# Performance work log

Hardware: AMD Instinct MI355X
Metric: run time of the kernel (lower is better)

Reference implementation:

```python
import jax, jax.numpy as jnp
import numpy as np

N, D, H, TOPK = 1024, 128, 8, 16
HD = D // H
EPS = 1e-5


def _linear_init(key, fan_in, fan_out):
    lim = 1.0 / np.sqrt(fan_in)
    kw, kb = jax.random.split(key)
    W = jax.random.uniform(kw, (fan_in, fan_out), minval=-lim, maxval=lim, dtype=jnp.float32)
    b = jax.random.uniform(kb, (fan_out,), minval=-lim, maxval=lim, dtype=jnp.float32)
    return W, b


def setup_inputs() -> dict:
    key = jax.random.key(0)
    ks = jax.random.split(key, 16)
    h = jax.random.normal(ks[0], (N, D), dtype=jnp.float32)
    e = jax.random.normal(ks[1], (N, N, D), dtype=jnp.float32)
    adjm_bin = jax.random.randint(ks[2], (N, N), 0, 2, dtype=jnp.int32)
    Wq, bq = _linear_init(ks[3], D, D)
    Wk, bk = _linear_init(ks[4], D, D)
    Wv, bv = _linear_init(ks[5], D, D)
    We, be = _linear_init(ks[6], D, H)
    Wo, bo = _linear_init(ks[7], D, D)
    Wf1, bf1 = _linear_init(ks[8], D, 4 * D)
    Wf2, bf2 = _linear_init(ks[9], 4 * D, D)
    # torch LSTMCell layout: W_ih [4D, D], W_hh [4D, D], gate order i,f,g,o
    lim = 1.0 / np.sqrt(D)
    Wih = jax.random.uniform(ks[10], (4 * D, D), minval=-lim, maxval=lim, dtype=jnp.float32)
    Whh = jax.random.uniform(ks[11], (4 * D, D), minval=-lim, maxval=lim, dtype=jnp.float32)
    bih = jax.random.uniform(ks[12], (4 * D,), minval=-lim, maxval=lim, dtype=jnp.float32)
    bhh = jax.random.uniform(ks[13], (4 * D,), minval=-lim, maxval=lim, dtype=jnp.float32)
    gn_g = jnp.ones((D,), jnp.float32); gn_b = jnp.zeros((D,), jnp.float32)
    ln1_g = jnp.ones((D,), jnp.float32); ln1_b = jnp.zeros((D,), jnp.float32)
    ln2_g = jnp.ones((D,), jnp.float32); ln2_b = jnp.zeros((D,), jnp.float32)
    return dict(h=h, e=e, adjm_bin=adjm_bin, Wq=Wq, bq=bq, Wk=Wk, bk=bk, Wv=Wv, bv=bv,
                We=We, be=be, Wo=Wo, bo=bo, Wf1=Wf1, bf1=bf1, Wf2=Wf2, bf2=bf2,
                Wih=Wih, Whh=Whh, bih=bih, bhh=bhh, gn_g=gn_g, gn_b=gn_b,
                ln1_g=ln1_g, ln1_b=ln1_b, ln2_g=ln2_g, ln2_b=ln2_b)


def _layernorm(x, g, b):
    mu = jnp.mean(x, axis=-1, keepdims=True)
    var = jnp.var(x, axis=-1, keepdims=True)
    return g * (x - mu) * jax.lax.rsqrt(var + EPS) + b


def _forward(h, e, Wq, bq, Wk, bk, Wv, bv, We, be, Wo, bo, Wf1, bf1, Wf2, bf2,
             Wih, Whh, bih, bhh, gn_g, gn_b, ln1_g, ln1_b, ln2_g, ln2_b):
    n = h.shape[0]
    residual = h
    q = (h @ Wq + bq).reshape(n, H, HD)
    k = (h @ Wk + bk).reshape(n, H, HD)
    v = (h @ Wv + bv).reshape(n, H, HD)
    scores = jnp.einsum('ihd,jhd->ijh', q, k) / np.sqrt(HD).astype(np.float32)
    scores = scores + (e @ We + be)                      # [N, N, H]
    # per-head top-k over neighbor dim j (axis=1)
    s = scores.transpose(0, 2, 1)                        # [N, H, N]
    _, idx = jax.lax.top_k(s, TOPK)                      # [N, H, K]
    mask = jnp.zeros(s.shape, bool).at[
        jnp.arange(n)[:, None, None], jnp.arange(H)[None, :, None], idx].set(True)
    mask = mask.transpose(0, 2, 1)                       # [N, N, H]
    scores = jnp.where(mask, scores, -jnp.inf)
    attn = jax.nn.softmax(scores, axis=1)
    h_attn = jnp.einsum('ijh,jhd->ihd', attn, v).reshape(n, D)
    h_attn = h_attn @ Wo + bo
    x = _layernorm(residual + h_attn, ln1_g, ln1_b)
    # LSTMCell with zero initial state (memory_state=None branch)
    gates = x @ Wih.T + bih + jnp.zeros_like(x) @ Whh.T + bhh
    gi, gf, gg, go = jnp.split(gates, 4, axis=-1)
    i = jax.nn.sigmoid(gi); f = jax.nn.sigmoid(gf)
    g = jnp.tanh(gg); o = jax.nn.sigmoid(go)
    c_next = i * g                                       # f * 0 dropped
    h_next = o * jnp.tanh(c_next)
    x = x + h_next
    # GraphNorm: normalize over node dim 0
    mu = jnp.mean(x, axis=0, keepdims=True)
    var = jnp.var(x, axis=0, keepdims=True)
    x = gn_g * (x - mu) * jax.lax.rsqrt(var + EPS) + gn_b
    h_ffn = jax.nn.relu(x @ Wf1 + bf1) @ Wf2 + bf2
    out = _layernorm(x + h_ffn, ln2_g, ln2_b)
    return out, h_next, c_next


def reference(h, e, adjm_bin, Wq, bq, Wk, bk, Wv, bv, We, be, Wo, bo, Wf1, bf1,
              Wf2, bf2, Wih, Whh, bih, bhh, gn_g, gn_b, ln1_g, ln1_b, ln2_g, ln2_b):
    # adjm_bin is accepted but unused, matching the original forward
    return _forward(h, e, Wq, bq, Wk, bk, Wv, bv, We, be, Wo, bo, Wf1, bf1,
                    Wf2, bf2, Wih, Whh, bih, bhh, gn_g, gn_b, ln1_g, ln1_b,
                    ln2_g, ln2_b)
```

## Files before the change

kernel.cpp:

```cpp
#include <hip/hip_runtime.h>
#include <math.h>
#include <float.h>
#include <stdint.h>

#define NN 1024
#define DD 128
#define HH 8
#define HDIM 16
#define KTOP 16
#define SCP 1032

typedef float vf4 __attribute__((ext_vector_type(4)));

__device__ __forceinline__ float wred_sum(float v) {
#pragma unroll
  for (int off = 32; off > 0; off >>= 1) v += __shfl_xor(v, off, 64);
  return v;
}

__device__ __forceinline__ float4 ntload4(const float* p) {
  vf4 r = __builtin_nontemporal_load((const vf4*)p);
  return make_float4(r.x, r.y, r.z, r.w);
}

template <int CTRL>
__device__ __forceinline__ float dpp_add(float v) {
  int x = __builtin_amdgcn_update_dpp(0, __float_as_int(v), CTRL, 0xF, 0xF, true);
  return v + __int_as_float(x);
}
#define DPP_XOR1 0xB1
#define DPP_XOR2 0x4E
#define DPP_ROR4 0x124
#define DPP_ROR8 0x128

__global__ __launch_bounds__(128) void k_qkv(
    const float* __restrict__ h,
    const float* __restrict__ Wq, const float* __restrict__ bq,
    const float* __restrict__ Wk, const float* __restrict__ bk,
    const float* __restrict__ Wv, const float* __restrict__ bv,
    float* __restrict__ q, float* __restrict__ k, float* __restrict__ v) {
  __shared__ float hrow[4][DD];
  const int t = threadIdx.x;
  const int i0 = blockIdx.x * 4;
#pragma unroll
  for (int r = 0; r < 4; ++r) hrow[r][t] = h[(i0 + r) * DD + t];
  __syncthreads();
  const float* W[3] = {Wq, Wk, Wv};
  const float* B[3] = {bq, bk, bv};
  float* O[3] = {q, k, v};
#pragma unroll
  for (int m = 0; m < 3; ++m) {
    float a0 = 0.f, a1 = 0.f, a2 = 0.f, a3 = 0.f;
    const float* Wm = W[m];
#pragma unroll 8
    for (int c = 0; c < DD; ++c) {
      float w = Wm[c * DD + t];
      a0 += hrow[0][c] * w; a1 += hrow[1][c] * w;
      a2 += hrow[2][c] * w; a3 += hrow[3][c] * w;
    }
    float b = B[m][t];
    float* Om = O[m];
    Om[(i0 + 0) * DD + t] = a0 + b;
    Om[(i0 + 1) * DD + t] = a1 + b;
    Om[(i0 + 2) * DD + t] = a2 + b;
    Om[(i0 + 3) * DD + t] = a3 + b;
  }
}

__global__ __launch_bounds__(128, 2) void k_attn(
    const float* __restrict__ e, const float* __restrict__ We, const float* __restrict__ be,
    const float* __restrict__ q, const float* __restrict__ kk, const float* __restrict__ v,
    float* __restrict__ hattn) {
  __shared__ float sc[HH * SCP];
  const int tid = threadIdx.x;
  const int lane = tid & 63;
  const int wv = tid >> 6;
  const int i = blockIdx.x;

  const int lrow = lane >> 4;
  const int c16 = lane & 15;
  const int c0 = c16 * 8;
  const int rb = wv * 8 + lrow;

  float4 w[16];
#pragma unroll
  for (int cl = 0; cl < 8; ++cl) {
    w[cl * 2]     = *(const float4*)(We + (c0 + cl) * HH);
    w[cl * 2 + 1] = *(const float4*)(We + (c0 + cl) * HH + 4);
  }
  float4 q0 = *(const float4*)(q + (size_t)i * DD + c0);
  float4 q1 = *(const float4*)(q + (size_t)i * DD + c0 + 4);
  q0.x *= 0.25f; q0.y *= 0.25f; q0.z *= 0.25f; q0.w *= 0.25f;
  q1.x *= 0.25f; q1.y *= 0.25f; q1.z *= 0.25f; q1.w *= 0.25f;
  const float behv = be[c16 >> 1];

  const float* ei = e + ((size_t)i << 17);
  const float* pa = ei + (size_t)rb * DD + c0;
  const float* pb = pa + 4 * DD;
  const float* ka = kk + (size_t)rb * DD + c0;
  const float* kb = ka + 4 * DD;

  float4 ea0 = ntload4(pa);          float4 ea1 = ntload4(pa + 4);
  float4 eb0 = ntload4(pb);          float4 eb1 = ntload4(pb + 4);
  float4 Ka0 = *(const float4*)(ka); float4 Ka1 = *(const float4*)(ka + 4);
  float4 Kb0 = *(const float4*)(kb); float4 Kb1 = *(const float4*)(kb + 4);

  for (int t = 0; t < 64; ++t) {
    float4 na0, na1, nb0, nb1, nKa0, nKa1, nKb0, nKb1;
    const bool more = (t + 1 < 64);
    if (more) {
      const float* xa = pa + (size_t)(t + 1) * (16 * DD);
      const float* xb = xa + 4 * DD;
      const float* ya = ka + (size_t)(t + 1) * (16 * DD);
      const float* yb = ya + 4 * DD;
      na0 = ntload4(xa);  na1 = ntload4(xa + 4);
      nb0 = ntload4(xb);  nb1 = ntload4(xb + 4);
      nKa0 = *(const float4*)(ya); nKa1 = *(const float4*)(ya + 4);
      nKb0 = *(const float4*)(yb); nKb1 = *(const float4*)(yb + 4);
    }

    float acca[8] = {0,0,0,0,0,0,0,0};
    float accb[8] = {0,0,0,0,0,0,0,0};
    const float eva[8] = {ea0.x, ea0.y, ea0.z, ea0.w, ea1.x, ea1.y, ea1.z, ea1.w};
    const float evb[8] = {eb0.x, eb0.y, eb0.z, eb0.w, eb1.x, eb1.y, eb1.z, eb1.w};
#pragma unroll
    for (int cl = 0; cl < 8; ++cl) {
      float4 wlo = w[cl * 2], whi = w[cl * 2 + 1];
      float a = eva[cl], b = evb[cl];
      acca[0] += a * wlo.x; acca[1] += a * wlo.y; acca[2] += a * wlo.z; acca[3] += a * wlo.w;
      acca[4] += a * whi.x; acca[5] += a * whi.y; acca[6] += a * whi.z; acca[7] += a * whi.w;
      accb[0] += b * wlo.x; accb[1] += b * wlo.y; accb[2] += b * wlo.z; accb[3] += b * wlo.w;
      accb[4] += b * whi.x; accb[5] += b * whi.y; accb[6] += b * whi.z; accb[7] += b * whi.w;
    }
    float qka = q0.x*Ka0.x + q0.y*Ka0.y + q0.z*Ka0.z + q0.w*Ka0.w
              + q1.x*Ka1.x + q1.y*Ka1.y + q1.z*Ka1.z + q1.w*Ka1.w;
    float qkb = q0.x*Kb0.x + q0.y*Kb0.y + q0.z*Kb0.z + q0.w*Kb0.w
              + q1.x*Kb1.x + q1.y*Kb1.y + q1.z*Kb1.z + q1.w*Kb1.w;

#pragma unroll
    for (int hh = 0; hh < 8; ++hh) {
      acca[hh] = dpp_add<DPP_XOR1>(acca[hh]);
      acca[hh] = dpp_add<DPP_XOR2>(acca[hh]);
      acca[hh] = dpp_add<DPP_ROR4>(acca[hh]);
      acca[hh] = dpp_add<DPP_ROR8>(acca[hh]);
      accb[hh] = dpp_add<DPP_XOR1>(accb[hh]);
      accb[hh] = dpp_add<DPP_XOR2>(accb[hh]);
      accb[hh] = dpp_add<DPP_ROR4>(accb[hh]);
      accb[hh] = dpp_add<DPP_ROR8>(accb[hh]);
    }
    qka = dpp_add<DPP_XOR1>(qka);
    qkb = dpp_add<DPP_XOR1>(qkb);

    if ((c16 & 1) == 0) {
      const int h = c16 >> 1;
      float sa = acca[0], sb = accb[0];
#pragma unroll
      for (int hh = 1; hh < 8; ++hh) {
        if (h == hh) { sa = acca[hh]; sb = accb[hh]; }
      }
      const int j = t * 16 + rb;
      sc[h * SCP + j]     = sa + qka + behv;
      sc[h * SCP + j + 4] = sb + qkb + behv;
    }

    if (more) {
      ea0 = na0; ea1 = na1; eb0 = nb0; eb1 = nb1;
      Ka0 = nKa0; Ka1 = nKa1; Kb0 = nKb0; Kb1 = nKb1;
    }
  }
  __syncthreads();

#pragma unroll 1
  for (int hp = 0; hp < 4; ++hp) {
    const int h = wv * 4 + hp;
    float val[16];
#pragma unroll
    for (int s = 0; s < 16; ++s) val[s] = sc[h * SCP + s * 64 + lane];
    int selj[16];
    float wgt[16];
    float vmax = 0.f, denom = 0.f;
#pragma unroll
    for (int t = 0; t < KTOP; ++t) {
      float bv = -FLT_MAX;
      int bj = 0x7FFFFFFF;
#pragma unroll
      for (int s = 0; s < 16; ++s) {
        float vs = val[s];
        int jj = s * 64 + lane;
        if (vs > bv) { bv = vs; bj = jj; }
      }
#pragma unroll
      for (int off = 32; off > 0; off >>= 1) {
        float ov = __shfl_xor(bv, off, 64);
        int oj = __shfl_xor(bj, off, 64);
        if (ov > bv || (ov == bv && oj < bj)) { bv = ov; bj = oj; }
      }
      selj[t] = bj;
      if (t == 0) vmax = bv;
      float wexp = expf(bv - vmax);
      wgt[t] = wexp;
      denom += wexp;
      const int so = bj >> 6;
      if ((bj & 63) == lane) {
#pragma unroll
        for (int s = 0; s < 16; ++s)
          if (s == so) val[s] = -FLT_MAX;
      }
    }
    const float inv = 1.0f / denom;
    const int d = lane & 15;
    float acc = 0.f;
#pragma unroll
    for (int t = 0; t < KTOP; ++t)
      acc += wgt[t] * v[(size_t)selj[t] * DD + h * HDIM + d];
    if (lane < 16) hattn[i * DD + h * HDIM + d] = acc * inv;
  }
}

__global__ __launch_bounds__(128) void k_post1(
    const float* __restrict__ h, const float* __restrict__ hattn,
    const float* __restrict__ Wo, const float* __restrict__ bo,
    const float* __restrict__ Wih, const float* __restrict__ bih, const float* __restrict__ bhh,
    const float* __restrict__ ln1g, const float* __restrict__ ln1b,
    float* __restrict__ x2, float* __restrict__ outh, float* __restrict__ outc) {
  __shared__ float arow[4][DD];
  __shared__ float x1s[4][DD];
  __shared__ float redS[4][2], redQ[4][2];
  const int t = threadIdx.x;
  const int i0 = blockIdx.x * 4;
#pragma unroll
  for (int r = 0; r < 4; ++r) arow[r][t] = hattn[(i0 + r) * DD + t];
  __syncthreads();
  float o0 = 0.f, o1 = 0.f, o2 = 0.f, o3 = 0.f;
#pragma unroll 4
  for (int c = 0; c < DD; ++c) {
    float w = Wo[c * DD + t];
    o0 += arow[0][c] * w; o1 += arow[1][c] * w;
    o2 += arow[2][c] * w; o3 += arow[3][c] * w;
  }
  float ovals[4] = {o0, o1, o2, o3};
  const float bov = bo[t], g1 = ln1g[t], b1 = ln1b[t];
#pragma unroll
  for (int r = 0; r < 4; ++r) {
    float res = h[(i0 + r) * DD + t] + ovals[r] + bov;
    float s1 = wred_sum(res), s2 = wred_sum(res * res);
    if ((t & 63) == 0) { redS[r][t >> 6] = s1; redQ[r][t >> 6] = s2; }
    __syncthreads();
    float mu = (redS[r][0] + redS[r][1]) * (1.f / 128.f);
    float var = (redQ[r][0] + redQ[r][1]) * (1.f / 128.f) - mu * mu;
    x1s[r][t] = g1 * (res - mu) * rsqrtf(var + 1e-5f) + b1;
  }
  __syncthreads();
  float gi[4] = {0, 0, 0, 0}, gg[4] = {0, 0, 0, 0}, go[4] = {0, 0, 0, 0};
  for (int c = 0; c < DD; ++c) {
    float wI = Wih[(t)*DD + c];
    float wG = Wih[(t + 256) * DD + c];
    float wO = Wih[(t + 384) * DD + c];
#pragma unroll
    for (int r = 0; r < 4; ++r) {
      float xv = x1s[r][c];
      gi[r] += xv * wI; gg[r] += xv * wG; go[r] += xv * wO;
    }
  }
  const float biI = bih[t] + bhh[t];
  const float biG = bih[t + 256] + bhh[t + 256];
  const float biO = bih[t + 384] + bhh[t + 384];
#pragma unroll
  for (int r = 0; r < 4; ++r) {
    float iv = 1.f / (1.f + expf(-(gi[r] + biI)));
    float gv = tanhf(gg[r] + biG);
    float ov = 1.f / (1.f + expf(-(go[r] + biO)));
    float cn = iv * gv;
    float hn = ov * tanhf(cn);
    outh[(i0 + r) * DD + t] = hn;
    outc[(i0 + r) * DD + t] = cn;
    x2[(i0 + r) * DD + t] = x1s[r][t] + hn;
  }
}

__global__ __launch_bounds__(256) void k_gncol(const float* __restrict__ x2,
                                               float* __restrict__ pS, float* __restrict__ pQ) {
  const int t = threadIdx.x, b = blockIdx.x;
  const int c = t & 127, half = t >> 7;
  const int r0 = b * 16 + half * 8;
  float s = 0.f, qq = 0.f;
#pragma unroll
  for (int r = 0; r < 8; ++r) {
    float v = x2[(r0 + r) * DD + c];
    s += v; qq += v * v;
  }
  pS[(b * 2 + half) * DD + c] = s;
  pQ[(b * 2 + half) * DD + c] = qq;
}

__global__ __launch_bounds__(128) void k_gnfin(const float* __restrict__ pS,
                                               const float* __restrict__ pQ,
                                               float* __restrict__ stats) {
  const int c = threadIdx.x;
  float s = 0.f, qq = 0.f;
#pragma unroll 8
  for (int kk = 0; kk < 128; ++kk) { s += pS[kk * DD + c]; qq += pQ[kk * DD + c]; }
  float mu = s * (1.f / 1024.f);
  float var = qq * (1.f / 1024.f) - mu * mu;
  stats[c] = mu;
  stats[DD + c] = rsqrtf(var + 1e-5f);
}

__global__ __launch_bounds__(256) void k_ffn(
    const float* __restrict__ x2, const float* __restrict__ stats,
    const float* __restrict__ gng, const float* __restrict__ gnb,
    const float* __restrict__ Wf1, const float* __restrict__ bf1,
    const float* __restrict__ Wf2, const float* __restrict__ bf2,
    const float* __restrict__ ln2g, const float* __restrict__ ln2b,
    float* __restrict__ out) {
  __shared__ float x3s[4][DD];
  __shared__ float hid[4][512];
  __shared__ float redC[4][256];
  __shared__ float redS[4][4], redQ[4][4];
  const int t = threadIdx.x;
  const int i0 = blockIdx.x * 4;
  for (int idx = t; idx < 4 * DD; idx += 256) {
    int r = idx >> 7, c = idx & 127;
    float vv = x2[(i0 + r) * DD + c];
    x3s[r][c] = gng[c] * (vv - stats[c]) * stats[DD + c] + gnb[c];
  }
  __syncthreads();
  {
    float a0[4] = {0, 0, 0, 0}, a1[4] = {0, 0, 0, 0};
#pragma unroll 2
    for (int c = 0; c < DD; ++c) {
      float w1 = Wf1[c * 512 + t];
      float w2 = Wf1[c * 512 + t + 256];
#pragma unroll
      for (int r = 0; r < 4; ++r) {
        float xv = x3s[r][c];
        a0[r] += xv * w1; a1[r] += xv * w2;
      }
    }
    float bb1 = bf1[t], bb2 = bf1[t + 256];
#pragma unroll
    for (int r = 0; r < 4; ++r) {
      hid[r][t] = fmaxf(a0[r] + bb1, 0.f);
      hid[r][t + 256] = fmaxf(a1[r] + bb2, 0.f);
    }
  }
  __syncthreads();
  const int d = t & 127, half = t >> 7;
  {
    float a[4] = {0, 0, 0, 0};
    for (int uu = 0; uu < 256; ++uu) {
      int u = half * 256 + uu;
      float w = Wf2[u * DD + d];
#pragma unroll
      for (int r = 0; r < 4; ++r) a[r] += hid[r][u] * w;
    }
#pragma unroll
    for (int r = 0; r < 4; ++r) redC[r][t] = a[r];
  }
  __syncthreads();
  const int lane = t & 63, wvv = t >> 6;
#pragma unroll 1
  for (int r = 0; r < 4; ++r) {
    float z = 0.f;
    if (t < DD) z = x3s[r][t] + redC[r][t] + redC[r][t + 128] + bf2[t];
    float s1 = wred_sum(z), s2 = wred_sum(z * z);
    if (lane == 0) { redS[r][wvv] = s1; redQ[r][wvv] = s2; }
    __syncthreads();
    float sum = redS[r][0] + redS[r][1] + redS[r][2] + redS[r][3];
    float sq = redQ[r][0] + redQ[r][1] + redQ[r][2] + redQ[r][3];
    float mu = sum * (1.f / 128.f);
    float var = sq * (1.f / 128.f) - mu * mu;
    float rs = rsqrtf(var + 1e-5f);
    if (t < DD) out[(i0 + r) * DD + t] = ln2g[t] * (z - mu) * rs + ln2b[t];
  }
}

extern "C" void kernel_launch(void* const* d_in, const int* in_sizes, int n_in,
                              void* d_out, int out_size, void* d_ws, size_t ws_size,
                              hipStream_t stream) {
  const float* h   = (const float*)d_in[0];
  const float* e   = (const float*)d_in[1];
  const float* Wq  = (const float*)d_in[3];
  const float* bq  = (const float*)d_in[4];
  const float* Wk  = (const float*)d_in[5];
  const float* bk  = (const float*)d_in[6];
  const float* Wv  = (const float*)d_in[7];
  const float* bv  = (const float*)d_in[8];
  const float* We  = (const float*)d_in[9];
  const float* be  = (const float*)d_in[10];
  const float* Wo  = (const float*)d_in[11];
  const float* bo  = (const float*)d_in[12];
  const float* Wf1 = (const float*)d_in[13];
  const float* bf1 = (const float*)d_in[14];
  const float* Wf2 = (const float*)d_in[15];
  const float* bf2 = (const float*)d_in[16];
  const float* Wih = (const float*)d_in[17];
  const float* bih = (const float*)d_in[19];
  const float* bhh = (const float*)d_in[20];
  const float* gng = (const float*)d_in[21];
  const float* gnb = (const float*)d_in[22];
  const float* l1g = (const float*)d_in[23];
  const float* l1b = (const float*)d_in[24];
  const float* l2g = (const float*)d_in[25];
  const float* l2b = (const float*)d_in[26];

  float* W = (float*)d_ws;
  float* q     = W;
  float* k     = W + 131072;
  float* v     = W + 262144;
  float* hattn = W + 393216;
  float* x2    = W + 524288;
  float* stats = W + 655360;
  float* pS    = W + 655616;
  float* pQ    = W + 672000;

  float* out  = (float*)d_out;
  float* outh = out + 131072;
  float* outc = out + 262144;

  hipLaunchKernelGGL(k_qkv, dim3(256), dim3(128), 0, stream,
                     h, Wq, bq, Wk, bk, Wv, bv, q, k, v);
  hipLaunchKernelGGL(k_attn, dim3(1024), dim3(128), 0, stream,
                     e, We, be, q, k, v, hattn);
  hipLaunchKernelGGL(k_post1, dim3(256), dim3(128), 0, stream,
                     h, hattn, Wo, bo, Wih, bih, bhh, l1g, l1b, x2, outh, outc);
  hipLaunchKernelGGL(k_gncol, dim3(64), dim3(256), 0, stream, x2, pS, pQ);
  hipLaunchKernelGGL(k_gnfin, dim3(1), dim3(128), 0, stream, pS, pQ, stats);
  hipLaunchKernelGGL(k_ffn, dim3(256), dim3(256), 0, stream,
                     x2, stats, gng, gnb, Wf1, bf1, Wf2, bf2, l2g, l2b, out);
}
```

Baseline: 226.5 us.

## Split attention into parallel score kernel and separate top-k kernel

The fused attention kernel is split in two. A score kernel runs over 8192 blocks of 256 threads, each handling a 128-column chunk of one row, and writes per-head scores to a global scratch buffer. A separate top-k kernel then reads those scores back to do selection and the value aggregation. This raises parallelism and occupancy for the bandwidth-bound pass over e (512MB), at the cost of a 32MB score round trip through global memory and an extra launch.

New measurement: 326.0 us. 1.44x slower.

```diff
diff --git a/kernel.cpp b/kernel.cpp
--- a/kernel.cpp
+++ b/kernel.cpp
@@ -8,7 +8,6 @@
 #define HH 8
 #define HDIM 16
 #define KTOP 16
-#define SCP 1032
 
 typedef float vf4 __attribute__((ext_vector_type(4)));
 
@@ -67,15 +66,16 @@
   }
 }
 
-__global__ __launch_bounds__(128, 2) void k_attn(
+__global__ __launch_bounds__(256, 3) void k_score(
     const float* __restrict__ e, const float* __restrict__ We, const float* __restrict__ be,
-    const float* __restrict__ q, const float* __restrict__ kk, const float* __restrict__ v,
-    float* __restrict__ hattn) {
-  __shared__ float sc[HH * SCP];
+    const float* __restrict__ q, const float* __restrict__ kk,
+    float* __restrict__ scG) {
   const int tid = threadIdx.x;
   const int lane = tid & 63;
   const int wv = tid >> 6;
-  const int i = blockIdx.x;
+  const int bid = blockIdx.x;
+  const int i = bid >> 3;
+  const int jc = bid & 7;
 
   const int lrow = lane >> 4;
   const int c16 = lane & 15;
@@ -94,30 +94,31 @@
   q1.x *= 0.25f; q1.y *= 0.25f; q1.z *= 0.25f; q1.w *= 0.25f;
   const float behv = be[c16 >> 1];
 
-  const float* ei = e + ((size_t)i << 17);
-  const float* pa = ei + (size_t)rb * DD + c0;
+  const int j0 = jc * 128;
+  const float* ebase = e + (size_t)i * (NN * DD) + (size_t)j0 * DD;
+  const float* pa = ebase + (size_t)rb * DD + c0;
   const float* pb = pa + 4 * DD;
-  const float* ka = kk + (size_t)rb * DD + c0;
+  const float* ka = kk + (size_t)(j0 + rb) * DD + c0;
   const float* kb = ka + 4 * DD;
+
+  float* scb = scG + (size_t)i * (HH * NN);
 
   float4 ea0 = ntload4(pa);          float4 ea1 = ntload4(pa + 4);
   float4 eb0 = ntload4(pb);          float4 eb1 = ntload4(pb + 4);
-  float4 Ka0 = *(const float4*)(ka); float4 Ka1 = *(const float4*)(ka + 4);
-  float4 Kb0 = *(const float4*)(kb); float4 Kb1 = *(const float4*)(kb + 4);
-
-  for (int t = 0; t < 64; ++t) {
-    float4 na0, na1, nb0, nb1, nKa0, nKa1, nKb0, nKb1;
-    const bool more = (t + 1 < 64);
+
+  for (int t = 0; t < 4; ++t) {
+    float4 na0, na1, nb0, nb1;
+    const bool more = (t + 1 < 4);
     if (more) {
-      const float* xa = pa + (size_t)(t + 1) * (16 * DD);
+      const float* xa = pa + (size_t)(t + 1) * (32 * DD);
       const float* xb = xa + 4 * DD;
-      const float* ya = ka + (size_t)(t + 1) * (16 * DD);
-      const float* yb = ya + 4 * DD;
       na0 = ntload4(xa);  na1 = ntload4(xa + 4);
       nb0 = ntload4(xb);  nb1 = ntload4(xb + 4);
-      nKa0 = *(const float4*)(ya); nKa1 = *(const float4*)(ya + 4);
-      nKb0 = *(const float4*)(yb); nKb1 = *(const float4*)(yb + 4);
-    }
+    }
+    const float* ya = ka + (size_t)t * (32 * DD);
+    const float* yb = ya + 4 * DD;
+    float4 Ka0 = *(const float4*)(ya); float4 Ka1 = *(const float4*)(ya + 4);
+    float4 Kb0 = *(const float4*)(yb); float4 Kb1 = *(const float4*)(yb + 4);
 
     float acca[8] = {0,0,0,0,0,0,0,0};
     float accb[8] = {0,0,0,0,0,0,0,0};
@@ -158,24 +159,30 @@
       for (int hh = 1; hh < 8; ++hh) {
         if (h == hh) { sa = acca[hh]; sb = accb[hh]; }
       }
-      const int j = t * 16 + rb;
-      sc[h * SCP + j]     = sa + qka + behv;
-      sc[h * SCP + j + 4] = sb + qkb + behv;
-    }
-
-    if (more) {
-      ea0 = na0; ea1 = na1; eb0 = nb0; eb1 = nb1;
-      Ka0 = nKa0; Ka1 = nKa1; Kb0 = nKb0; Kb1 = nKb1;
-    }
-  }
-  __syncthreads();
+      const int j = j0 + t * 32 + rb;
+      scb[h * NN + j]     = sa + qka + behv;
+      scb[h * NN + j + 4] = sb + qkb + behv;
+    }
+
+    if (more) { ea0 = na0; ea1 = na1; eb0 = nb0; eb1 = nb1; }
+  }
+}
+
+__global__ __launch_bounds__(128) void k_topk(
+    const float* __restrict__ scG, const float* __restrict__ v,
+    float* __restrict__ hattn) {
+  const int tid = threadIdx.x;
+  const int lane = tid & 63;
+  const int wv = tid >> 6;
+  const int i = blockIdx.x;
+  const float* scb = scG + (size_t)i * (HH * NN);
 
 #pragma unroll 1
   for (int hp = 0; hp < 4; ++hp) {
     const int h = wv * 4 + hp;
     float val[16];
 #pragma unroll
-    for (int s = 0; s < 16; ++s) val[s] = sc[h * SCP + s * 64 + lane];
+    for (int s = 0; s < 16; ++s) val[s] = scb[h * NN + s * 64 + lane];
     int selj[16];
     float wgt[16];
     float vmax = 0.f, denom = 0.f;
@@ -413,6 +420,7 @@
   float* stats = W + 655360;
   float* pS    = W + 655616;
   float* pQ    = W + 672000;
+  float* scG   = W + 1048576;
 
   float* out  = (float*)d_out;
   float* outh = out + 131072;
@@ -420,8 +428,10 @@
 
   hipLaunchKernelGGL(k_qkv, dim3(256), dim3(128), 0, stream,
                      h, Wq, bq, Wk, bk, Wv, bv, q, k, v);
-  hipLaunchKernelGGL(k_attn, dim3(1024), dim3(128), 0, stream,
-                     e, We, be, q, k, v, hattn);
+  hipLaunchKernelGGL(k_score, dim3(8192), dim3(256), 0, stream,
+                     e, We, be, q, k, scG);
+  hipLaunchKernelGGL(k_topk, dim3(1024), dim3(128), 0, stream,
+                     scG, v, hattn);
   hipLaunchKernelGGL(k_post1, dim3(256), dim3(128), 0, stream,
                      h, hattn, Wo, bo, Wih, bih, bhh, l1g, l1b, x2, outh, outc);
   hipLaunchKernelGGL(k_gncol, dim3(64), dim3(256), 0, stream, x2, pS, pQ);
```

## Precompute QK attention scores in a separate tiled kernel before edge pass

Applied to the files above, without the earlier changes.

Moves the per-head q·k score computation out of the edge-streaming attention kernel into a new register-tiled kernel that writes all head scores to a global scratch buffer. The attention kernel then preloads the scores into shared memory and only adds the edge projection, so its main loop no longer streams K rows or does the dot products. This trades an extra launch and a 32 MB scores write and read for a lighter loop in the e-bandwidth-bound kernel.

Result: slower. 246.4 us (+8.8%).

```diff
diff --git a/kernel.cpp b/kernel.cpp
--- a/kernel.cpp
+++ b/kernel.cpp
@@ -67,9 +67,56 @@
   }
 }
 
+__global__ __launch_bounds__(256) void k_qk(
+    const float* __restrict__ q, const float* __restrict__ kk,
+    const float* __restrict__ be, float* __restrict__ scG) {
+  __shared__ float qs[16 * 64];
+  __shared__ float ks[16 * 64];
+  const int t = threadIdx.x;
+  const int i0 = blockIdx.x * 64;
+  const int j0 = blockIdx.y * 64;
+  const int h = blockIdx.z;
+
+  {
+    const int il = t >> 2;
+    const int dq = (t & 3) * 4;
+    float4 qv = *(const float4*)(q + (size_t)(i0 + il) * DD + h * HDIM + dq);
+    qs[(dq + 0) * 64 + il] = qv.x * 0.25f;
+    qs[(dq + 1) * 64 + il] = qv.y * 0.25f;
+    qs[(dq + 2) * 64 + il] = qv.z * 0.25f;
+    qs[(dq + 3) * 64 + il] = qv.w * 0.25f;
+    float4 kv = *(const float4*)(kk + (size_t)(j0 + il) * DD + h * HDIM + dq);
+    ks[(dq + 0) * 64 + il] = kv.x;
+    ks[(dq + 1) * 64 + il] = kv.y;
+    ks[(dq + 2) * 64 + il] = kv.z;
+    ks[(dq + 3) * 64 + il] = kv.w;
+  }
+  __syncthreads();
+
+  const int ti = t & 15;
+  const int tj = t >> 4;
+  float acc[4][4] = {{0,0,0,0},{0,0,0,0},{0,0,0,0},{0,0,0,0}};
+#pragma unroll
+  for (int d = 0; d < 16; ++d) {
+    float4 qv = *(const float4*)&qs[d * 64 + ti * 4];
+    float4 kv = *(const float4*)&ks[d * 64 + tj * 4];
+    acc[0][0] += qv.x * kv.x; acc[0][1] += qv.x * kv.y; acc[0][2] += qv.x * kv.z; acc[0][3] += qv.x * kv.w;
+    acc[1][0] += qv.y * kv.x; acc[1][1] += qv.y * kv.y; acc[1][2] += qv.y * kv.z; acc[1][3] += qv.y * kv.w;
+    acc[2][0] += qv.z * kv.x; acc[2][1] += qv.z * kv.y; acc[2][2] += qv.z * kv.z; acc[2][3] += qv.z * kv.w;
+    acc[3][0] += qv.w * kv.x; acc[3][1] += qv.w * kv.y; acc[3][2] += qv.w * kv.z; acc[3][3] += qv.w * kv.w;
+  }
+  const float beh = be[h];
+#pragma unroll
+  for (int a = 0; a < 4; ++a) {
+    float4 st = make_float4(acc[a][0] + beh, acc[a][1] + beh,
+                            acc[a][2] + beh, acc[a][3] + beh);
+    *(float4*)(scG + (size_t)(i0 + ti * 4 + a) * (HH * NN) + h * NN + j0 + tj * 4) = st;
+  }
+}
+
 __global__ __launch_bounds__(128, 2) void k_attn(
-    const float* __restrict__ e, const float* __restrict__ We, const float* __restrict__ be,
-    const float* __restrict__ q, const float* __restrict__ kk, const float* __restrict__ v,
+    const float* __restrict__ e, const float* __restrict__ We,
+    const float* __restrict__ scG, const float* __restrict__ v,
     float* __restrict__ hattn) {
   __shared__ float sc[HH * SCP];
   const int tid = threadIdx.x;
@@ -82,41 +129,37 @@
   const int c0 = c16 * 8;
   const int rb = wv * 8 + lrow;
 
+  const float* ei = e + ((size_t)i << 17);
+  const float* pa = ei + (size_t)rb * DD + c0;
+  const float* pb = pa + 4 * DD;
+
+  float4 ea0 = ntload4(pa);          float4 ea1 = ntload4(pa + 4);
+  float4 eb0 = ntload4(pb);          float4 eb1 = ntload4(pb + 4);
+
   float4 w[16];
 #pragma unroll
   for (int cl = 0; cl < 8; ++cl) {
     w[cl * 2]     = *(const float4*)(We + (c0 + cl) * HH);
     w[cl * 2 + 1] = *(const float4*)(We + (c0 + cl) * HH + 4);
   }
-  float4 q0 = *(const float4*)(q + (size_t)i * DD + c0);
-  float4 q1 = *(const float4*)(q + (size_t)i * DD + c0 + 4);
-  q0.x *= 0.25f; q0.y *= 0.25f; q0.z *= 0.25f; q0.w *= 0.25f;
-  q1.x *= 0.25f; q1.y *= 0.25f; q1.z *= 0.25f; q1.w *= 0.25f;
-  const float behv = be[c16 >> 1];
-
-  const float* ei = e + ((size_t)i << 17);
-  const float* pa = ei + (size_t)rb * DD + c0;
-  const float* pb = pa + 4 * DD;
-  const float* ka = kk + (size_t)rb * DD + c0;
-  const float* kb = ka + 4 * DD;
-
-  float4 ea0 = ntload4(pa);          float4 ea1 = ntload4(pa + 4);
-  float4 eb0 = ntload4(pb);          float4 eb1 = ntload4(pb + 4);
-  float4 Ka0 = *(const float4*)(ka); float4 Ka1 = *(const float4*)(ka + 4);
-  float4 Kb0 = *(const float4*)(kb); float4 Kb1 = *(const float4*)(kb + 4);
+
+  {
+    const float* scb = scG + (size_t)i * (HH * NN);
+    for (int f = tid; f < 2048; f += 128) {
+      int h = f >> 8, j4 = f & 255;
+      *(float4*)&sc[h * SCP + j4 * 4] = *(const float4*)&scb[h * NN + j4 * 4];
+    }
+  }
+  __syncthreads();
 
   for (int t = 0; t < 64; ++t) {
-    float4 na0, na1, nb0, nb1, nKa0, nKa1, nKb0, nKb1;
+    float4 na0, na1, nb0, nb1;
     const bool more = (t + 1 < 64);
     if (more) {
       const float* xa = pa + (size_t)(t + 1) * (16 * DD);
       const float* xb = xa + 4 * DD;
-      const float* ya = ka + (size_t)(t + 1) * (16 * DD);
-      const float* yb = ya + 4 * DD;
       na0 = ntload4(xa);  na1 = ntload4(xa + 4);
       nb0 = ntload4(xb);  nb1 = ntload4(xb + 4);
-      nKa0 = *(const float4*)(ya); nKa1 = *(const float4*)(ya + 4);
-      nKb0 = *(const float4*)(yb); nKb1 = *(const float4*)(yb + 4);
     }
 
     float acca[8] = {0,0,0,0,0,0,0,0};
@@ -132,10 +175,6 @@
       accb[0] += b * wlo.x; accb[1] += b * wlo.y; accb[2] += b * wlo.z; accb[3] += b * wlo.w;
       accb[4] += b * whi.x; accb[5] += b * whi.y; accb[6] += b * whi.z; accb[7] += b * whi.w;
     }
-    float qka = q0.x*Ka0.x + q0.y*Ka0.y + q0.z*Ka0.z + q0.w*Ka0.w
-              + q1.x*Ka1.x + q1.y*Ka1.y + q1.z*Ka1.z + q1.w*Ka1.w;
-    float qkb = q0.x*Kb0.x + q0.y*Kb0.y + q0.z*Kb0.z + q0.w*Kb0.w
-              + q1.x*Kb1.x + q1.y*Kb1.y + q1.z*Kb1.z + q1.w*Kb1.w;
 
 #pragma unroll
     for (int hh = 0; hh < 8; ++hh) {
@@ -148,8 +187,6 @@
       accb[hh] = dpp_add<DPP_ROR4>(accb[hh]);
       accb[hh] = dpp_add<DPP_ROR8>(accb[hh]);
     }
-    qka = dpp_add<DPP_XOR1>(qka);
-    qkb = dpp_add<DPP_XOR1>(qkb);
 
     if ((c16 & 1) == 0) {
       const int h = c16 >> 1;
@@ -159,14 +196,11 @@
         if (h == hh) { sa = acca[hh]; sb = accb[hh]; }
       }
       const int j = t * 16 + rb;
-      sc[h * SCP + j]     = sa + qka + behv;
-      sc[h * SCP + j + 4] = sb + qkb + behv;
-    }
-
-    if (more) {
-      ea0 = na0; ea1 = na1; eb0 = nb0; eb1 = nb1;
-      Ka0 = nKa0; Ka1 = nKa1; Kb0 = nKb0; Kb1 = nKb1;
-    }
+      sc[h * SCP + j]     += sa;
+      sc[h * SCP + j + 4] += sb;
+    }
+
+    if (more) { ea0 = na0; ea1 = na1; eb0 = nb0; eb1 = nb1; }
   }
   __syncthreads();
 
@@ -413,6 +447,7 @@
   float* stats = W + 655360;
   float* pS    = W + 655616;
   float* pQ    = W + 672000;
+  float* scG   = W + 1048576;
 
   float* out  = (float*)d_out;
   float* outh = out + 131072;
@@ -420,8 +455,10 @@
 
   hipLaunchKernelGGL(k_qkv, dim3(256), dim3(128), 0, stream,
                      h, Wq, bq, Wk, bk, Wv, bv, q, k, v);
+  hipLaunchKernelGGL(k_qk, dim3(16, 16, 8), dim3(256), 0, stream,
+                     q, k, be, scG);
   hipLaunchKernelGGL(k_attn, dim3(1024), dim3(128), 0, stream,
-                     e, We, be, q, k, v, hattn);
+                     e, We, scG, v, hattn);
   hipLaunchKernelGGL(k_post1, dim3(256), dim3(128), 0, stream,
                      h, hattn, Wo, bo, Wih, bih, bhh, l1g, l1b, x2, outh, outc);
   hipLaunchKernelGGL(k_gncol, dim3(64), dim3(256), 0, stream, x2, pS, pQ);
```
